# Kernel tuning notes

Measured on AMD Instinct MI355X. Metric: run time of the kernel, lower is better.

Reference implementation:

```python
import jax, jax.numpy as jnp
import numpy as np


def setup_inputs() -> dict:
    key = jax.random.key(0)
    k1, k2, k3 = jax.random.split(key, 3)
    B, T, N, D = 16, 12, 4096, 64
    M = 128  # memory_num
    return {
        "nodevec1": jax.random.normal(k1, (B, T, N, D), dtype=jnp.float32),
        "nodevec2": jax.random.normal(k2, (B, T, N, D), dtype=jnp.float32),
        "node_embeddings": jax.random.normal(k3, (M, 2 * D), dtype=jnp.float32),
        "topk": 32,
    }


def reference(nodevec1, nodevec2, node_embeddings, topk):
    B, T, N, D = nodevec1.shape
    M = node_embeddings.shape[0]
    # nodevec3: [B,T,N,2D] matches node_embeddings' 2*time_dim trailing dim
    nodevec3 = jnp.concatenate([nodevec1, nodevec2], axis=-1)
    # attention-like map over nodes: [B,T,M,N]
    logits = jnp.einsum('me,btne->btmn', node_embeddings, nodevec3)
    supports2 = jax.nn.softmax(logits, axis=-1)
    values, indices = jax.lax.top_k(supports2, topk)  # [B,T,M,K], sorted desc

    def gather(x):
        # gather K nodes per memory slot along the N axis
        idx = indices.reshape(B, T, M * topk, 1)  # [B,T,M*K,1]
        g = jnp.take_along_axis(x, idx, axis=2)   # [B,T,M*K,D]
        return g.reshape(B, T, M, topk, D)

    sel1 = gather(nodevec1)
    sel2 = gather(nodevec2)
    batch_indices = jnp.broadcast_to(jnp.arange(B).reshape(B, 1, 1, 1), (B, T, M, topk))
    time_indices = jnp.broadcast_to(jnp.arange(T).reshape(1, T, 1, 1), (B, T, M, topk))
    return (sel1, sel2, batch_indices, time_indices, indices)
```

## Files before the change

### kernel.cpp

```cpp
#include <hip/hip_runtime.h>
#include <stdint.h>

typedef unsigned long long u64;
typedef unsigned short u16;
typedef __attribute__((ext_vector_type(8))) short short8;
typedef __attribute__((ext_vector_type(4))) float f32x4;

#define NB   16
#define NT   12
#define BTc  192
#define NN   4096
#define DD   64
#define MM   128
#define TOPK 32
#define KTH  36
#define CAP  128

#define SEL1_OFF 0ULL
#define SEL2_OFF 50331648ULL
#define BIDX_OFF 100663296ULL
#define TIDX_OFF 101449728ULL
#define IDX_OFF  102236160ULL

__device__ __forceinline__ unsigned ord32(float f) {
    unsigned u = __float_as_uint(f);
    return (u & 0x80000000u) ? ~u : (u | 0x80000000u);
}
__device__ __forceinline__ u16 f2bf(float f) {
    unsigned u = __float_as_uint(f);
    unsigned r = u + 0x7FFFu + ((u >> 16) & 1u);
    return (u16)(r >> 16);
}
__device__ __forceinline__ float bf2f(short s) {
    return __uint_as_float(((unsigned)(u16)s) << 16);
}
__device__ __forceinline__ u64 pack4bf(float4 v) {
    return (u64)f2bf(v.x) | ((u64)f2bf(v.y) << 16) |
           ((u64)f2bf(v.z) << 32) | ((u64)f2bf(v.w) << 48);
}
__device__ __forceinline__ void lds_fence() {
    asm volatile("s_waitcnt lgkmcnt(0)" ::: "memory");
    __builtin_amdgcn_sched_barrier(0);
}
__device__ __forceinline__ u64 sort64_desc(u64 v, int l) {
#pragma unroll
    for (int k = 2; k <= 64; k <<= 1) {
#pragma unroll
        for (int j = k >> 1; j >= 1; j >>= 1) {
            u64 o = __shfl_xor(v, j);
            bool takeMax = (((l & j) == 0) == ((l & k) == 0));
            v = takeMax ? (v > o ? v : o) : (v < o ? v : o);
        }
    }
    return v;
}

__global__ __launch_bounds__(256) void k1_logits_bf16(const float* __restrict__ nv1,
                                                      const float* __restrict__ nv2,
                                                      const float* __restrict__ emb,
                                                      u16* __restrict__ logitsB) {
    __shared__ u16 Als[128 * 128];
    __shared__ u16 Bls[128 * 128];

    const int tid = threadIdx.x;
    const int nt  = blockIdx.x;
    const int bt  = blockIdx.y;
    const int n0  = nt * 128;

#pragma unroll
    for (int it = 0; it < 16; ++it) {
        int f4  = it * 256 + tid;
        int row = f4 >> 5;
        int kq  = f4 & 31;
        float4 a = *(const float4*)(emb + row * 128 + kq * 4);
        int byte = row * 256 + ((kq * 8) ^ ((row & 7) << 4));
        *(u64*)((char*)Als + byte) = pack4bf(a);
    }
#pragma unroll
    for (int it = 0; it < 16; ++it) {
        int f4  = it * 256 + tid;
        int row = f4 >> 5;
        int kq  = f4 & 31;
        const float* src = (kq < 16)
            ? (nv1 + ((size_t)bt * NN + n0 + row) * DD + kq * 4)
            : (nv2 + ((size_t)bt * NN + n0 + row) * DD + (kq - 16) * 4);
        float4 bv = *(const float4*)src;
        int byte = row * 256 + ((kq * 8) ^ ((row & 7) << 4));
        *(u64*)((char*)Bls + byte) = pack4bf(bv);
    }
    __syncthreads();

    const int w  = tid >> 6;
    const int l  = tid & 63;
    const int mb = (w >> 1) * 64;
    const int nb = (w & 1) * 64;
    const int xr = (l & 7) << 4;

    f32x4 acc[4][4];
#pragma unroll
    for (int mi = 0; mi < 4; ++mi)
#pragma unroll
        for (int ni = 0; ni < 4; ++ni) acc[mi][ni] = {0.f, 0.f, 0.f, 0.f};

#pragma unroll
    for (int ks = 0; ks < 4; ++ks) {
        const int kb = (ks * 64 + (l >> 4) * 16) ^ xr;
        short8 a[4], b[4];
#pragma unroll
        for (int mi = 0; mi < 4; ++mi) {
            int row = mb + mi * 16 + (l & 15);
            a[mi] = *(const short8*)((const char*)Als + row * 256 + kb);
        }
#pragma unroll
        for (int ni = 0; ni < 4; ++ni) {
            int row = nb + ni * 16 + (l & 15);
            b[ni] = *(const short8*)((const char*)Bls + row * 256 + kb);
        }
#pragma unroll
        for (int mi = 0; mi < 4; ++mi)
#pragma unroll
            for (int ni = 0; ni < 4; ++ni)
                acc[mi][ni] = __builtin_amdgcn_mfma_f32_16x16x32_bf16(
                    a[mi], b[ni], acc[mi][ni], 0, 0, 0);
    }

    const size_t rbase = (size_t)bt * MM * NN;
#pragma unroll
    for (int mi = 0; mi < 4; ++mi)
#pragma unroll
        for (int ni = 0; ni < 4; ++ni) {
            int n = n0 + nb + ni * 16 + (l & 15);
#pragma unroll
            for (int r = 0; r < 4; ++r) {
                int m = mb + mi * 16 + (l >> 4) * 4 + r;
                logitsB[rbase + (size_t)m * NN + n] = f2bf(acc[mi][ni][r]);
            }
        }
}

__global__ __launch_bounds__(256) void k2_fused(const u16* logitsB,
                                                const float* __restrict__ nv1,
                                                const float* __restrict__ nv2,
                                                const float* __restrict__ emb,
                                                float* out) {
    const int tid = threadIdx.x;
    const int l   = tid & 63;
    const int w   = tid >> 6;
    const int bid = (int)blockIdx.x;
    const int swz = (bid & 7) * 768 + (bid >> 3);
    const int row = swz * 4 + w;
    const int bt  = row >> 7;
    const int m   = row & 127;
    const u16* src = logitsB + (size_t)row * NN;

    __shared__ int   cand[4][CAP];
    __shared__ float embrow[4][128];

    embrow[w][l]      = emb[m * 128 + l];
    embrow[w][l + 64] = emb[m * 128 + 64 + l];

    short8 ch[8];
    float lmax = -INFINITY;
#pragma unroll
    for (int j = 0; j < 8; ++j) {
        ch[j] = *(const short8*)(src + j * 512 + l * 8);
#pragma unroll
        for (int e = 0; e < 8; ++e) lmax = fmaxf(lmax, bf2f(ch[j][e]));
    }

    float v = lmax;
#pragma unroll
    for (int k = 2; k <= 64; k <<= 1) {
#pragma unroll
        for (int j = k >> 1; j >= 1; j >>= 1) {
            float o = __shfl_xor(v, j);
            bool takeMax = (((l & j) == 0) == ((l & k) == 0));
            v = takeMax ? fmaxf(v, o) : fminf(v, o);
        }
    }
    const float T = __shfl(v, KTH - 1);

    int c = 0;
#pragma unroll
    for (int j = 0; j < 8; ++j) {
#pragma unroll
        for (int e = 0; e < 8; ++e) {
            bool p = (bf2f(ch[j][e]) >= T);
            u64 mask = __ballot(p);
            if (p) {
                int pos = c + (int)__popcll(mask & ((1ull << l) - 1ull));
                if (pos < CAP) cand[w][pos] = j * 512 + l * 8 + e;
            }
            c += (int)__popcll(mask);
        }
    }
    if (c > CAP) c = CAP;
    lds_fence();

    u64 kreg[2] = {0ull, 0ull};
    const int nch = (c + 63) >> 6;
    for (int s3 = 0; s3 < nch; ++s3) {
        int s = s3 * 64 + l;
        if (s < c) {
            int n = cand[w][s];
            const float4* c1 = (const float4*)(nv1 + ((size_t)bt * NN + n) * DD);
            const float4* c2 = (const float4*)(nv2 + ((size_t)bt * NN + n) * DD);
            float4 r[16];
            float acc = 0.f;
#pragma unroll
            for (int q = 0; q < 16; ++q) r[q] = c1[q];
#pragma unroll
            for (int q = 0; q < 16; ++q) {
                acc = fmaf(embrow[w][q * 4 + 0], r[q].x, acc);
                acc = fmaf(embrow[w][q * 4 + 1], r[q].y, acc);
                acc = fmaf(embrow[w][q * 4 + 2], r[q].z, acc);
                acc = fmaf(embrow[w][q * 4 + 3], r[q].w, acc);
            }
#pragma unroll
            for (int q = 0; q < 16; ++q) r[q] = c2[q];
#pragma unroll
            for (int q = 0; q < 16; ++q) {
                acc = fmaf(embrow[w][64 + q * 4 + 0], r[q].x, acc);
                acc = fmaf(embrow[w][64 + q * 4 + 1], r[q].y, acc);
                acc = fmaf(embrow[w][64 + q * 4 + 2], r[q].z, acc);
                acc = fmaf(embrow[w][64 + q * 4 + 3], r[q].w, acc);
            }
            kreg[s3] = ((u64)ord32(acc) << 32) | (u64)(0xFFFFFFFFu - (unsigned)n);
        }
    }

    u64 top = sort64_desc(kreg[0], l);
    if (c > 64) {
        u64 B = sort64_desc(kreg[1], l);
        u64 rb = __shfl_xor(B, 63);
        u64 M = top > rb ? top : rb;
#pragma unroll
        for (int j = 32; j >= 1; j >>= 1) {
            u64 o = __shfl_xor(M, j);
            M = ((l & j) == 0) ? (M > o ? M : o) : (M < o ? M : o);
        }
        top = M;
    }

    const int b = bt / NT;
    const int t = bt - b * NT;
    const size_t obase = (size_t)row * TOPK;
    const unsigned mynode = 0xFFFFFFFFu - (unsigned)(top & 0xFFFFFFFFull);
    if (l < TOPK) {
        out[IDX_OFF  + obase + l] = (float)mynode;
        out[BIDX_OFF + obase + l] = (float)b;
        out[TIDX_OFF + obase + l] = (float)t;
    }

    int myn[8];
#pragma unroll
    for (int it = 0; it < 8; ++it) {
        int p = it * 4 + (l >> 4);
        u64 kk = __shfl(top, p);
        myn[it] = (int)(0xFFFFFFFFu - (unsigned)(kk & 0xFFFFFFFFull)) & (NN - 1);
    }
    const int j4 = (l & 15) * 4;
    float4 s1[8], s2[8];
#pragma unroll
    for (int it = 0; it < 8; ++it)
        s1[it] = *(const float4*)(nv1 + ((size_t)bt * NN + myn[it]) * DD + j4);
#pragma unroll
    for (int it = 0; it < 8; ++it)
        s2[it] = *(const float4*)(nv2 + ((size_t)bt * NN + myn[it]) * DD + j4);
#pragma unroll
    for (int it = 0; it < 8; ++it) {
        int p = it * 4 + (l >> 4);
        size_t o = (obase + p) * DD + j4;
        *(float4*)(out + SEL1_OFF + o) = s1[it];
        *(float4*)(out + SEL2_OFF + o) = s2[it];
    }
}

extern "C" void kernel_launch(void* const* d_in, const int* in_sizes, int n_in,
                              void* d_out, int out_size, void* d_ws, size_t ws_size,
                              hipStream_t stream) {
    const float* nv1 = (const float*)d_in[0];
    const float* nv2 = (const float*)d_in[1];
    const float* emb = (const float*)d_in[2];
    float* out = (float*)d_out;

    dim3 g1(32, BTc);
    k1_logits_bf16<<<g1, 256, 0, stream>>>(nv1, nv2, emb, (u16*)d_out);
    k2_fused<<<24576 / 4, 256, 0, stream>>>((const u16*)d_out, nv1, nv2, emb, out);
}
```

Measured before the change: 410.1 us.

## Emit per-group logit maxima in k1 and scan only candidate groups in k2

The logits kernel now also writes the bf16 maximum of each 32-column group per row into scratch space inside the output buffer. The selection kernel merges the two sorted halves of these 128 group maxima to find a threshold, then reads and ballots only the groups whose maximum reaches it, instead of streaming the full 4096-entry logit row. The goal is to cut k2's global reads and compare work per row. It adds extra shuffles and stores in k1, raises KTH to 44 to keep enough candidates, and removes some register staging of loads, which may lower memory-level parallelism.

New measurement: 447.0 us. 9.0% more time.

```diff
diff --git a/kernel.cpp b/kernel.cpp
--- a/kernel.cpp
+++ b/kernel.cpp
@@ -13,7 +13,7 @@
 #define DD   64
 #define MM   128
 #define TOPK 32
-#define KTH  36
+#define KTH  44
 #define CAP  128
 
 #define SEL1_OFF 0ULL
@@ -42,6 +42,18 @@
     asm volatile("s_waitcnt lgkmcnt(0)" ::: "memory");
     __builtin_amdgcn_sched_barrier(0);
 }
+__device__ __forceinline__ float sort64f_desc(float v, int l) {
+#pragma unroll
+    for (int k = 2; k <= 64; k <<= 1) {
+#pragma unroll
+        for (int j = k >> 1; j >= 1; j >>= 1) {
+            float o = __shfl_xor(v, j);
+            bool takeMax = (((l & j) == 0) == ((l & k) == 0));
+            v = takeMax ? fmaxf(v, o) : fminf(v, o);
+        }
+    }
+    return v;
+}
 __device__ __forceinline__ u64 sort64_desc(u64 v, int l) {
 #pragma unroll
     for (int k = 2; k <= 64; k <<= 1) {
@@ -58,7 +70,8 @@
 __global__ __launch_bounds__(256) void k1_logits_bf16(const float* __restrict__ nv1,
                                                       const float* __restrict__ nv2,
                                                       const float* __restrict__ emb,
-                                                      u16* __restrict__ logitsB) {
+                                                      float* __restrict__ outBase) {
+    u16* logitsB = (u16*)outBase;
     __shared__ u16 Als[128 * 128];
     __shared__ u16 Bls[128 * 128];
 
@@ -136,6 +149,29 @@
                 logitsB[rbase + (size_t)m * NN + n] = f2bf(acc[mi][ni][r]);
             }
         }
+
+    u16* sum_lo = (u16*)((char*)outBase + BIDX_OFF * 4);
+    u16* sum_hi = (u16*)((char*)outBase + TIDX_OFF * 4);
+#pragma unroll
+    for (int mi = 0; mi < 4; ++mi)
+#pragma unroll
+        for (int pr = 0; pr < 2; ++pr)
+#pragma unroll
+            for (int r = 0; r < 4; ++r) {
+                float v = fmaxf(bf2f((short)f2bf(acc[mi][pr * 2][r])),
+                                bf2f((short)f2bf(acc[mi][pr * 2 + 1][r])));
+#pragma unroll
+                for (int mk = 1; mk < 16; mk <<= 1)
+                    v = fmaxf(v, __shfl_xor(v, mk));
+                if ((l & 15) == 0) {
+                    int m   = mb + mi * 16 + (l >> 4) * 4 + r;
+                    int g   = nt * 4 + (nb >> 5) + pr;
+                    int rw  = bt * MM + m;
+                    u16 hv  = f2bf(v);
+                    if (g < 64) sum_lo[rw * 64 + g]        = hv;
+                    else        sum_hi[rw * 64 + (g - 64)] = hv;
+                }
+            }
 }
 
 __global__ __launch_bounds__(256) void k2_fused(const u16* logitsB,
@@ -154,42 +190,56 @@
     const u16* src = logitsB + (size_t)row * NN;
 
     __shared__ int   cand[4][CAP];
+    __shared__ int   glist[4][128];
     __shared__ float embrow[4][128];
 
     embrow[w][l]      = emb[m * 128 + l];
     embrow[w][l + 64] = emb[m * 128 + 64 + l];
 
-    short8 ch[8];
-    float lmax = -INFINITY;
-#pragma unroll
-    for (int j = 0; j < 8; ++j) {
-        ch[j] = *(const short8*)(src + j * 512 + l * 8);
-#pragma unroll
-        for (int e = 0; e < 8; ++e) lmax = fmaxf(lmax, bf2f(ch[j][e]));
-    }
-
-    float v = lmax;
-#pragma unroll
-    for (int k = 2; k <= 64; k <<= 1) {
-#pragma unroll
-        for (int j = k >> 1; j >= 1; j >>= 1) {
-            float o = __shfl_xor(v, j);
-            bool takeMax = (((l & j) == 0) == ((l & k) == 0));
-            v = takeMax ? fmaxf(v, o) : fminf(v, o);
-        }
-    }
-    const float T = __shfl(v, KTH - 1);
+    const u16* sum_lo = (const u16*)((const char*)out + BIDX_OFF * 4) + row * 64;
+    const u16* sum_hi = (const u16*)((const char*)out + TIDX_OFF * 4) + row * 64;
+    const float gm0 = bf2f((short)sum_lo[l]);
+    const float gm1 = bf2f((short)sum_hi[l]);
+
+    const float A = sort64f_desc(gm0, l);
+    const float B = sort64f_desc(gm1, l);
+    const float INF = __builtin_inff();
+    float av = __shfl(A, (l >= 1) ? l - 1 : 0);
+    if (l < 1) av = INF;
+    int jb = KTH - 1 - l;
+    float bv = __shfl(B, (jb >= 0 && jb < 64) ? jb : 0);
+    if (jb < 0) bv = INF;
+    float mm = (l <= KTH) ? fminf(av, bv) : -INF;
+#pragma unroll
+    for (int mk = 1; mk < 64; mk <<= 1)
+        mm = fmaxf(mm, __shfl_xor(mm, mk));
+    const float T = mm;
+
+    u64 m0 = __ballot(gm0 >= T);
+    u64 m1 = __ballot(gm1 >= T);
+    const u64 below = (1ull << l) - 1ull;
+    const int n0q = (int)__popcll(m0);
+    if (gm0 >= T) glist[w][__popcll(m0 & below)] = l;
+    if (gm1 >= T) glist[w][n0q + (int)__popcll(m1 & below)] = 64 + l;
+    const int ng = n0q + (int)__popcll(m1);
+    lds_fence();
 
     int c = 0;
-#pragma unroll
-    for (int j = 0; j < 8; ++j) {
+    const int rounds = (ng + 15) >> 4;
+    for (int rd = 0; rd < rounds; ++rd) {
+        int gi = rd * 16 + (l >> 2);
+        bool act = gi < ng;
+        int g = act ? glist[w][gi] : 0;
+        short8 v8 = {0, 0, 0, 0, 0, 0, 0, 0};
+        if (act) v8 = *(const short8*)(src + g * 32 + (l & 3) * 8);
+        int nbase = g * 32 + (l & 3) * 8;
 #pragma unroll
         for (int e = 0; e < 8; ++e) {
-            bool p = (bf2f(ch[j][e]) >= T);
+            bool p = act && (bf2f(v8[e]) >= T);
             u64 mask = __ballot(p);
             if (p) {
-                int pos = c + (int)__popcll(mask & ((1ull << l) - 1ull));
-                if (pos < CAP) cand[w][pos] = j * 512 + l * 8 + e;
+                int pos = c + (int)__popcll(mask & below);
+                if (pos < CAP) cand[w][pos] = nbase + e;
             }
             c += (int)__popcll(mask);
         }
@@ -205,25 +255,22 @@
             int n = cand[w][s];
             const float4* c1 = (const float4*)(nv1 + ((size_t)bt * NN + n) * DD);
             const float4* c2 = (const float4*)(nv2 + ((size_t)bt * NN + n) * DD);
-            float4 r[16];
             float acc = 0.f;
 #pragma unroll
-            for (int q = 0; q < 16; ++q) r[q] = c1[q];
-#pragma unroll
             for (int q = 0; q < 16; ++q) {
-                acc = fmaf(embrow[w][q * 4 + 0], r[q].x, acc);
-                acc = fmaf(embrow[w][q * 4 + 1], r[q].y, acc);
-                acc = fmaf(embrow[w][q * 4 + 2], r[q].z, acc);
-                acc = fmaf(embrow[w][q * 4 + 3], r[q].w, acc);
-            }
-#pragma unroll
-            for (int q = 0; q < 16; ++q) r[q] = c2[q];
+                float4 x = c1[q];
+                acc = fmaf(embrow[w][q * 4 + 0], x.x, acc);
+                acc = fmaf(embrow[w][q * 4 + 1], x.y, acc);
+                acc = fmaf(embrow[w][q * 4 + 2], x.z, acc);
+                acc = fmaf(embrow[w][q * 4 + 3], x.w, acc);
+            }
 #pragma unroll
             for (int q = 0; q < 16; ++q) {
-                acc = fmaf(embrow[w][64 + q * 4 + 0], r[q].x, acc);
-                acc = fmaf(embrow[w][64 + q * 4 + 1], r[q].y, acc);
-                acc = fmaf(embrow[w][64 + q * 4 + 2], r[q].z, acc);
-                acc = fmaf(embrow[w][64 + q * 4 + 3], r[q].w, acc);
+                float4 x = c2[q];
+                acc = fmaf(embrow[w][64 + q * 4 + 0], x.x, acc);
+                acc = fmaf(embrow[w][64 + q * 4 + 1], x.y, acc);
+                acc = fmaf(embrow[w][64 + q * 4 + 2], x.z, acc);
+                acc = fmaf(embrow[w][64 + q * 4 + 3], x.w, acc);
             }
             kreg[s3] = ((u64)ord32(acc) << 32) | (u64)(0xFFFFFFFFu - (unsigned)n);
         }
@@ -231,8 +278,8 @@
 
     u64 top = sort64_desc(kreg[0], l);
     if (c > 64) {
-        u64 B = sort64_desc(kreg[1], l);
-        u64 rb = __shfl_xor(B, 63);
+        u64 Bk = sort64_desc(kreg[1], l);
+        u64 rb = __shfl_xor(Bk, 63);
         u64 M = top > rb ? top : rb;
 #pragma unroll
         for (int j = 32; j >= 1; j >>= 1) {
@@ -260,19 +307,14 @@
         myn[it] = (int)(0xFFFFFFFFu - (unsigned)(kk & 0xFFFFFFFFull)) & (NN - 1);
     }
     const int j4 = (l & 15) * 4;
-    float4 s1[8], s2[8];
-#pragma unroll
-    for (int it = 0; it < 8; ++it)
-        s1[it] = *(const float4*)(nv1 + ((size_t)bt * NN + myn[it]) * DD + j4);
-#pragma unroll
-    for (int it = 0; it < 8; ++it)
-        s2[it] = *(const float4*)(nv2 + ((size_t)bt * NN + myn[it]) * DD + j4);
 #pragma unroll
     for (int it = 0; it < 8; ++it) {
         int p = it * 4 + (l >> 4);
+        const float4 s1 = *(const float4*)(nv1 + ((size_t)bt * NN + myn[it]) * DD + j4);
+        const float4 s2 = *(const float4*)(nv2 + ((size_t)bt * NN + myn[it]) * DD + j4);
         size_t o = (obase + p) * DD + j4;
-        *(float4*)(out + SEL1_OFF + o) = s1[it];
-        *(float4*)(out + SEL2_OFF + o) = s2[it];
+        *(float4*)(out + SEL1_OFF + o) = s1;
+        *(float4*)(out + SEL2_OFF + o) = s2;
     }
 }
 
@@ -285,6 +327,6 @@
     float* out = (float*)d_out;
 
     dim3 g1(32, BTc);
-    k1_logits_bf16<<<g1, 256, 0, stream>>>(nv1, nv2, emb, (u16*)d_out);
+    k1_logits_bf16<<<g1, 256, 0, stream>>>(nv1, nv2, emb, out);
     k2_fused<<<24576 / 4, 256, 0, stream>>>((const u16*)d_out, nv1, nv2, emb, out);
 }
```
